# Kernel optimization log

Hardware: AMD Instinct MI355X
Metric: run time of the kernel (lower is better)

## Reference

```python
import jax, jax.numpy as jnp
import numpy as np

DIM = 1024
HEADS = 16
SCALE = DIM ** -0.5  # NOTE: original scales by full dim, not head dim


def setup_inputs() -> dict:
    key = jax.random.key(0)
    ks = jax.random.split(key, 6)
    B, S, D = 2, 2048, DIM
    x = jax.random.normal(ks[0], (B, S, D), dtype=jnp.float32)
    Wq = jax.random.normal(ks[1], (D, D), dtype=jnp.float32) * 0.02
    Wk = jax.random.normal(ks[2], (D, D), dtype=jnp.float32) * 0.02
    Wv = jax.random.normal(ks[3], (D, D), dtype=jnp.float32) * 0.02
    Wo = jax.random.normal(ks[4], (D, D), dtype=jnp.float32) * 0.02
    z = jnp.zeros((D,), dtype=jnp.float32)
    return {"x": x, "Wq": Wq, "bq": z, "Wk": Wk, "bk": z, "Wv": Wv, "bv": z, "Wo": Wo, "bo": z}


def reference(x, Wq, bq, Wk, bk, Wv, bv, Wo, bo):
    B, S, D = x.shape
    H = HEADS
    d = D // H
    # projections (Linear: x @ W + b)
    q = (x @ Wq + bq).reshape(B, S, H, d).transpose(0, 2, 1, 3)  # b h i d
    k = (x @ Wk + bk).reshape(B, S, H, d).transpose(0, 2, 1, 3)  # b h j d
    v = (x @ Wv + bv).reshape(B, S, H, d).transpose(0, 2, 1, 3)  # b h j d
    dots = jnp.einsum("bhid,bhjd->bhij", q, k) * SCALE
    # causal mask: strict upper triangle -> -inf
    mask = jnp.triu(jnp.ones((S, S), dtype=bool), k=1)
    dots = jnp.where(mask, -jnp.inf, dots)
    attn = jax.nn.softmax(dots, axis=-1)
    out = jnp.einsum("bhij,bhjd->bhid", attn, v)
    out = out.transpose(0, 2, 1, 3).reshape(B, S, D)  # b i (h d)
    return out @ Wo + bo
```

## Files before the change

### kernel.cpp

```cpp
#include <hip/hip_runtime.h>
#include <hip/hip_bf16.h>

typedef __bf16 bf16;
typedef __bf16 bf16x4 __attribute__((ext_vector_type(4)));
typedef __bf16 bf16x8 __attribute__((ext_vector_type(8)));
typedef float floatx4 __attribute__((ext_vector_type(4)));

#define MFMA_16x16x32(a, b, c) __builtin_amdgcn_mfma_f32_16x16x32_bf16((a), (b), (c), 0, 0, 0)
#define NEG_INF (-__builtin_inff())

#define CB 2
#define CS 2048
#define CD 1024
#define CH 16
#define CM (CB * CS)
#define QSC (0.03125f * 1.44269504088896340736f)

__device__ __forceinline__ void async16(const bf16* g, bf16* l) {
    __builtin_amdgcn_global_load_lds(
        (const __attribute__((address_space(1))) void*)g,
        (__attribute__((address_space(3))) void*)l, 16, 0, 0);
}

__global__ __launch_bounds__(256) void conv_x(const float* __restrict__ x,
                                              bf16* __restrict__ xb) {
    size_t i = ((size_t)blockIdx.x * 256 + threadIdx.x) * 8;
    float4 a = *(const float4*)(x + i);
    float4 b = *(const float4*)(x + i + 4);
    bf16x8 v;
    v[0] = (bf16)a.x; v[1] = (bf16)a.y; v[2] = (bf16)a.z; v[3] = (bf16)a.w;
    v[4] = (bf16)b.x; v[5] = (bf16)b.y; v[6] = (bf16)b.z; v[7] = (bf16)b.w;
    *(bf16x8*)(xb + i) = v;
}

__global__ __launch_bounds__(256) void conv_wt(
    const float* __restrict__ W0, const float* __restrict__ W1,
    const float* __restrict__ W2, const float* __restrict__ W3,
    bf16* __restrict__ Wt) {
    __shared__ bf16 Ws[64 * 68];
    const float* W = blockIdx.z == 0 ? W0 : blockIdx.z == 1 ? W1
                   : blockIdx.z == 2 ? W2 : W3;
    bf16* out = Wt + (size_t)blockIdx.z * CD * CD;
    const int t = threadIdx.x;
    const int n0 = blockIdx.x * 64, k0 = blockIdx.y * 64;
    const int rr = t >> 4, c4 = (t & 15) * 4;
#pragma unroll
    for (int i = 0; i < 4; i++) {
        int r = rr + i * 16;
        float4 f = *(const float4*)(W + (size_t)(k0 + r) * CD + n0 + c4);
        bf16x4 v;
        v[0] = (bf16)f.x; v[1] = (bf16)f.y; v[2] = (bf16)f.z; v[3] = (bf16)f.w;
        *(bf16x4*)&Ws[r * 68 + c4] = v;
    }
    __syncthreads();
#pragma unroll
    for (int i = 0; i < 4; i++) {
        int n = rr + i * 16;
        bf16x4 v;
#pragma unroll
        for (int j = 0; j < 4; j++) v[j] = Ws[(c4 + j) * 68 + n];
        *(bf16x4*)(out + (size_t)(n0 + n) * CD + k0 + c4) = v;
    }
}

__global__ __launch_bounds__(256) void gemm_qkv(
    const bf16* __restrict__ A, const bf16* __restrict__ Bt,
    const float* __restrict__ bq, const float* __restrict__ bk,
    const float* __restrict__ bv,
    bf16* __restrict__ Qb, bf16* __restrict__ Kb, bf16* __restrict__ Vb) {
    __shared__ bf16 As[128 * 32];
    __shared__ bf16 Bs[128 * 32];
    const int t = threadIdx.x, w = t >> 6, lane = t & 63;
    const int quad = lane >> 4, l15 = lane & 15;
    const int which = blockIdx.x >> 3;
    const int bn = (blockIdx.x & 7) * 128, bm = blockIdx.y * 128;
    const bf16* Bw = Bt + (size_t)which * CD * CD;

    const bf16* ag = A + (size_t)(bm + w * 16 + (lane >> 2)) * CD + (lane & 3) * 8;
    const bf16* bg = Bw + (size_t)(bn + w * 16 + (lane >> 2)) * CD + (lane & 3) * 8;
    const int lo = w * 16 * 32;

    const int wm = (w >> 1) * 64, wn = (w & 1) * 64;
    floatx4 acc[4][4] = {};

    for (int k0 = 0; k0 < CD; k0 += 32) {
        async16(ag + k0, &As[lo]);
        async16(ag + (size_t)64 * CD + k0, &As[lo + 64 * 32]);
        async16(bg + k0, &Bs[lo]);
        async16(bg + (size_t)64 * CD + k0, &Bs[lo + 64 * 32]);
        __syncthreads();
        bf16x8 af[4], bfr[4];
#pragma unroll
        for (int mt = 0; mt < 4; mt++)
            af[mt] = *(const bf16x8*)&As[(wm + mt * 16 + l15) * 32 + quad * 8];
#pragma unroll
        for (int nt = 0; nt < 4; nt++)
            bfr[nt] = *(const bf16x8*)&Bs[(wn + nt * 16 + l15) * 32 + quad * 8];
#pragma unroll
        for (int mt = 0; mt < 4; mt++)
#pragma unroll
            for (int nt = 0; nt < 4; nt++)
                acc[mt][nt] = MFMA_16x16x32(af[mt], bfr[nt], acc[mt][nt]);
        __syncthreads();
    }

    const float* bias = which == 0 ? bq : which == 1 ? bk : bv;
    bf16* out = which == 0 ? Qb : Kb;
#pragma unroll
    for (int mt = 0; mt < 4; mt++) {
#pragma unroll
        for (int nt = 0; nt < 4; nt++) {
            int token = bm + wm + mt * 16 + quad * 4;
            int col = bn + wn + nt * 16 + l15;
            int b = token >> 11, s = token & (CS - 1);
            int h = col >> 6, dd = col & 63;
            if (which == 2) {
                bf16x4 pv;
#pragma unroll
                for (int r = 0; r < 4; r++) pv[r] = (bf16)(acc[mt][nt][r] + bias[col]);
                *(bf16x4*)&Vb[(((size_t)(b * CH + h)) * 64 + dd) * CS + s] = pv;
            } else {
#pragma unroll
                for (int r = 0; r < 4; r++) {
                    float v = acc[mt][nt][r] + bias[col];
                    if (which == 0) v *= QSC;
                    out[(((size_t)(b * CH + h)) * CS + s + r) * 64 + dd] = (bf16)v;
                }
            }
        }
    }
}

__global__ __launch_bounds__(256) void gemm_o(
    const bf16* __restrict__ A, const bf16* __restrict__ Bt,
    const float* __restrict__ bias, float* __restrict__ out) {
    __shared__ bf16 As[64 * 32];
    __shared__ bf16 Bs[128 * 32];
    const int t = threadIdx.x, w = t >> 6, lane = t & 63;
    const int quad = lane >> 4, l15 = lane & 15;
    const int bn = blockIdx.x * 128, bm = blockIdx.y * 64;

    const bf16* ag = A + (size_t)(bm + w * 16 + (lane >> 2)) * CD + (lane & 3) * 8;
    const bf16* bg = Bt + (size_t)(bn + w * 16 + (lane >> 2)) * CD + (lane & 3) * 8;
    const int lo = w * 16 * 32;

    const int wm = (w >> 1) * 32, wn = (w & 1) * 64;
    floatx4 acc[2][4] = {};

    for (int k0 = 0; k0 < CD; k0 += 32) {
        async16(ag + k0, &As[lo]);
        async16(bg + k0, &Bs[lo]);
        async16(bg + (size_t)64 * CD + k0, &Bs[lo + 64 * 32]);
        __syncthreads();
        bf16x8 af[2], bfr[4];
#pragma unroll
        for (int mt = 0; mt < 2; mt++)
            af[mt] = *(const bf16x8*)&As[(wm + mt * 16 + l15) * 32 + quad * 8];
#pragma unroll
        for (int nt = 0; nt < 4; nt++)
            bfr[nt] = *(const bf16x8*)&Bs[(wn + nt * 16 + l15) * 32 + quad * 8];
#pragma unroll
        for (int mt = 0; mt < 2; mt++)
#pragma unroll
            for (int nt = 0; nt < 4; nt++)
                acc[mt][nt] = MFMA_16x16x32(af[mt], bfr[nt], acc[mt][nt]);
        __syncthreads();
    }

#pragma unroll
    for (int mt = 0; mt < 2; mt++)
#pragma unroll
        for (int nt = 0; nt < 4; nt++)
#pragma unroll
            for (int r = 0; r < 4; r++) {
                int row = bm + wm + mt * 16 + quad * 4 + r;
                int col = bn + wn + nt * 16 + l15;
                out[(size_t)row * CD + col] = acc[mt][nt][r] + bias[col];
            }
}

__global__ __launch_bounds__(256) void attn_kernel(
    const bf16* __restrict__ Q, const bf16* __restrict__ Kg,
    const bf16* __restrict__ Vg, bf16* __restrict__ Ob) {
    __shared__ bf16 Ks[64 * 72];
    __shared__ bf16 Vt[64 * 72];
    __shared__ bf16 Pt[4][32 * 72];

    const int t = threadIdx.x;
    const int w = t >> 6, lane = t & 63;
    const int quad = lane >> 4, l15 = lane & 15;

    const int half = blockIdx.x >> 8;
    const int slot = blockIdx.x & 255;
    const int bh   = slot & 31;
    const int qq   = slot >> 5;
    const int qb   = half ? qq : (15 - qq);
    const int q0   = qb * 128;
    const int wrow0 = q0 + w * 32;
    const int nT = 2 * qb + 2;

    const bf16* Qh = Q + (size_t)bh * CS * 64;
    const bf16* Kh = Kg + (size_t)bh * CS * 64;
    const bf16* Vh = Vg + (size_t)bh * 64 * CS;

    const int strow = t >> 2, soff = (t & 3) * 16;
    const bf16* ksrc = Kh + (size_t)strow * 64 + soff;
    const bf16* vsrc = Vh + (size_t)strow * CS + soff;

    bf16x8 kr0 = *(const bf16x8*)ksrc;
    bf16x8 kr1 = *(const bf16x8*)(ksrc + 8);
    bf16x8 vr0 = *(const bf16x8*)vsrc;
    bf16x8 vr1 = *(const bf16x8*)(vsrc + 8);

    bf16x8 qf[2][2];
#pragma unroll
    for (int g = 0; g < 2; g++) {
        const bf16* qsrc = Qh + (size_t)(wrow0 + g * 16 + l15) * 64 + quad * 8;
        qf[g][0] = *(const bf16x8*)qsrc;
        qf[g][1] = *(const bf16x8*)(qsrc + 32);
    }

    floatx4 o[4][2] = {};
    float m_r[2] = {NEG_INF, NEG_INF}, l_r[2] = {0.f, 0.f};

    bf16* pw = Pt[w];

    for (int kt = 0; kt < nT; kt++) {
        const int ks0 = kt * 64;
        __syncthreads();
        *(bf16x8*)&Ks[strow * 72 + soff]     = kr0;
        *(bf16x8*)&Ks[strow * 72 + soff + 8] = kr1;
        *(bf16x8*)&Vt[strow * 72 + soff]     = vr0;
        *(bf16x8*)&Vt[strow * 72 + soff + 8] = vr1;
        __syncthreads();
        {
            int nk = (kt + 1 < nT) ? kt + 1 : 0;
            const bf16* kn = ksrc + (size_t)nk * 64 * 64;
            const bf16* vn = vsrc + nk * 64;
            kr0 = *(const bf16x8*)kn;
            kr1 = *(const bf16x8*)(kn + 8);
            vr0 = *(const bf16x8*)vn;
            vr1 = *(const bf16x8*)(vn + 8);
        }
        if (ks0 > wrow0 + 31) continue;

        floatx4 sc[2][4] = {};
#pragma unroll
        for (int nt = 0; nt < 4; nt++) {
            bf16x8 af0 = *(const bf16x8*)&Ks[(nt * 16 + l15) * 72 + quad * 8];
            bf16x8 af1 = *(const bf16x8*)&Ks[(nt * 16 + l15) * 72 + 32 + quad * 8];
#pragma unroll
            for (int g = 0; g < 2; g++) {
                sc[g][nt] = MFMA_16x16x32(af0, qf[g][0], sc[g][nt]);
                sc[g][nt] = MFMA_16x16x32(af1, qf[g][1], sc[g][nt]);
            }
        }
        if (ks0 + 63 > wrow0) {
#pragma unroll
            for (int g = 0; g < 2; g++) {
                int qrow = wrow0 + g * 16 + l15;
#pragma unroll
                for (int nt = 0; nt < 4; nt++)
#pragma unroll
                    for (int r = 0; r < 4; r++)
                        if (ks0 + nt * 16 + quad * 4 + r > qrow)
                            sc[g][nt][r] = NEG_INF;
            }
        }
        float alpha_g[2];
#pragma unroll
        for (int g = 0; g < 2; g++) {
            float mx = NEG_INF;
#pragma unroll
            for (int nt = 0; nt < 4; nt++)
#pragma unroll
                for (int r = 0; r < 4; r++) mx = fmaxf(mx, sc[g][nt][r]);
            mx = fmaxf(mx, __shfl_xor(mx, 16));
            mx = fmaxf(mx, __shfl_xor(mx, 32));
            float mn = fmaxf(m_r[g], mx);
            alpha_g[g] = __builtin_amdgcn_exp2f(m_r[g] - mn);
            m_r[g] = mn;
            float sum = 0.f;
#pragma unroll
            for (int nt = 0; nt < 4; nt++)
#pragma unroll
                for (int r = 0; r < 4; r++) {
                    sc[g][nt][r] = __builtin_amdgcn_exp2f(sc[g][nt][r] - mn);
                    sum += sc[g][nt][r];
                }
            sum += __shfl_xor(sum, 16);
            sum += __shfl_xor(sum, 32);
            l_r[g] = l_r[g] * alpha_g[g] + sum;
        }
#pragma unroll
        for (int g = 0; g < 2; g++)
#pragma unroll
            for (int nt = 0; nt < 4; nt++) {
                bf16x4 pk;
#pragma unroll
                for (int r = 0; r < 4; r++) pk[r] = (bf16)sc[g][nt][r];
                *(bf16x4*)&pw[(g * 16 + l15) * 72 + nt * 16 + quad * 4] = pk;
            }
        bf16x8 bp[2][2];
#pragma unroll
        for (int g = 0; g < 2; g++) {
            bp[g][0] = *(const bf16x8*)&pw[(g * 16 + l15) * 72 + quad * 8];
            bp[g][1] = *(const bf16x8*)&pw[(g * 16 + l15) * 72 + 32 + quad * 8];
        }
#pragma unroll
        for (int dt = 0; dt < 4; dt++)
#pragma unroll
            for (int g = 0; g < 2; g++)
#pragma unroll
                for (int r = 0; r < 4; r++) o[dt][g][r] *= alpha_g[g];
#pragma unroll
        for (int dt = 0; dt < 4; dt++) {
            bf16x8 av0 = *(const bf16x8*)&Vt[(dt * 16 + l15) * 72 + quad * 8];
            bf16x8 av1 = *(const bf16x8*)&Vt[(dt * 16 + l15) * 72 + 32 + quad * 8];
#pragma unroll
            for (int g = 0; g < 2; g++) {
                o[dt][g] = MFMA_16x16x32(av0, bp[g][0], o[dt][g]);
                o[dt][g] = MFMA_16x16x32(av1, bp[g][1], o[dt][g]);
            }
        }
    }

    const int b = bh >> 4, h = bh & 15;
#pragma unroll
    for (int g = 0; g < 2; g++) {
        float rl = 1.f / l_r[g];
        int row = wrow0 + g * 16 + l15;
#pragma unroll
        for (int dt = 0; dt < 4; dt++) {
            bf16x4 ov;
#pragma unroll
            for (int r = 0; r < 4; r++) ov[r] = (bf16)(o[dt][g][r] * rl);
            *(bf16x4*)&Ob[((size_t)b * CS + row) * CD + h * 64 + dt * 16 + quad * 4] = ov;
        }
    }
}

extern "C" void kernel_launch(void* const* d_in, const int* in_sizes, int n_in,
                              void* d_out, int out_size, void* d_ws, size_t ws_size,
                              hipStream_t stream) {
    const float* x  = (const float*)d_in[0];
    const float* Wq = (const float*)d_in[1];
    const float* bq = (const float*)d_in[2];
    const float* Wk = (const float*)d_in[3];
    const float* bk = (const float*)d_in[4];
    const float* Wv = (const float*)d_in[5];
    const float* bv = (const float*)d_in[6];
    const float* Wo = (const float*)d_in[7];
    const float* bo = (const float*)d_in[8];
    float* out = (float*)d_out;

    bf16* xb = (bf16*)d_ws;
    bf16* Wt = xb + (size_t)CM * CD;
    bf16* Qb = Wt + (size_t)4 * CD * CD;
    bf16* Kb = Qb + (size_t)CB * CH * CS * 64;
    bf16* Vb = Kb + (size_t)CB * CH * CS * 64;
    bf16* Ob = Vb + (size_t)CB * CH * CS * 64;

    conv_x<<<(CM * CD) / (256 * 8), 256, 0, stream>>>(x, xb);
    conv_wt<<<dim3(CD / 64, CD / 64, 4), 256, 0, stream>>>(Wq, Wk, Wv, Wo, Wt);

    gemm_qkv<<<dim3(24, CM / 128), 256, 0, stream>>>(
        xb, Wt, bq, bk, bv, Qb, Kb, Vb);

    attn_kernel<<<512, 256, 0, stream>>>(Qb, Kb, Vb, Ob);

    gemm_o<<<dim3(8, CM / 64), 256, 0, stream>>>(
        Ob, Wt + (size_t)3 * CD * CD, bo, out);
}
```

Before: 194.4 us.

## Load attention K/V fragments directly into registers and vectorize GEMM epilogues

The attention kernel stops staging K and V tiles in shared memory with block-wide barriers. Each wave now loads its own MFMA fragments straight from global memory into registers, prefetching the next tile, and runs only up to its own causal limit. This removes the __syncthreads and lets waves proceed independently, at the cost of more redundant global/L2 traffic because every wave reloads the same K/V. The QKV and output GEMMs swap the MFMA operand order so the epilogue can write contiguous 4-element vectors with float4 bias loads, and the attention kernel gets a launch_bounds occupancy hint of 2.

```diff
diff --git a/kernel.cpp b/kernel.cpp
--- a/kernel.cpp
+++ b/kernel.cpp
@@ -75,6 +75,7 @@
     const int which = blockIdx.x >> 3;
     const int bn = (blockIdx.x & 7) * 128, bm = blockIdx.y * 128;
     const bf16* Bw = Bt + (size_t)which * CD * CD;
+    const bool vpath = (which == 2);
 
     const bf16* ag = A + (size_t)(bm + w * 16 + (lane >> 2)) * CD + (lane & 3) * 8;
     const bf16* bg = Bw + (size_t)(bn + w * 16 + (lane >> 2)) * CD + (lane & 3) * 8;
@@ -96,38 +97,57 @@
 #pragma unroll
         for (int nt = 0; nt < 4; nt++)
             bfr[nt] = *(const bf16x8*)&Bs[(wn + nt * 16 + l15) * 32 + quad * 8];
+        if (vpath) {
+#pragma unroll
+            for (int mt = 0; mt < 4; mt++)
+#pragma unroll
+                for (int nt = 0; nt < 4; nt++)
+                    acc[mt][nt] = MFMA_16x16x32(af[mt], bfr[nt], acc[mt][nt]);
+        } else {
+#pragma unroll
+            for (int mt = 0; mt < 4; mt++)
+#pragma unroll
+                for (int nt = 0; nt < 4; nt++)
+                    acc[mt][nt] = MFMA_16x16x32(bfr[nt], af[mt], acc[mt][nt]);
+        }
+        __syncthreads();
+    }
+
+    if (vpath) {
 #pragma unroll
         for (int mt = 0; mt < 4; mt++)
 #pragma unroll
-            for (int nt = 0; nt < 4; nt++)
-                acc[mt][nt] = MFMA_16x16x32(af[mt], bfr[nt], acc[mt][nt]);
-        __syncthreads();
-    }
-
-    const float* bias = which == 0 ? bq : which == 1 ? bk : bv;
-    bf16* out = which == 0 ? Qb : Kb;
-#pragma unroll
-    for (int mt = 0; mt < 4; mt++) {
-#pragma unroll
-        for (int nt = 0; nt < 4; nt++) {
-            int token = bm + wm + mt * 16 + quad * 4;
-            int col = bn + wn + nt * 16 + l15;
-            int b = token >> 11, s = token & (CS - 1);
-            int h = col >> 6, dd = col & 63;
-            if (which == 2) {
+            for (int nt = 0; nt < 4; nt++) {
+                int token = bm + wm + mt * 16 + quad * 4;
+                int col = bn + wn + nt * 16 + l15;
+                int b = token >> 11, s = token & (CS - 1);
+                int h = col >> 6, dd = col & 63;
                 bf16x4 pv;
 #pragma unroll
-                for (int r = 0; r < 4; r++) pv[r] = (bf16)(acc[mt][nt][r] + bias[col]);
+                for (int r = 0; r < 4; r++) pv[r] = (bf16)(acc[mt][nt][r] + bv[col]);
                 *(bf16x4*)&Vb[(((size_t)(b * CH + h)) * 64 + dd) * CS + s] = pv;
-            } else {
+            }
+    } else {
+        const float* bias = which == 0 ? bq : bk;
+        bf16* out = which == 0 ? Qb : Kb;
+#pragma unroll
+        for (int mt = 0; mt < 4; mt++)
+#pragma unroll
+            for (int nt = 0; nt < 4; nt++) {
+                int token = bm + wm + mt * 16 + l15;
+                int f = bn + wn + nt * 16 + quad * 4;
+                int b = token >> 11, s = token & (CS - 1);
+                int h = f >> 6, dd = f & 63;
+                float4 bb = *(const float4*)(bias + f);
+                bf16x4 pv;
 #pragma unroll
                 for (int r = 0; r < 4; r++) {
-                    float v = acc[mt][nt][r] + bias[col];
+                    float v = acc[mt][nt][r] + ((const float*)&bb)[r];
                     if (which == 0) v *= QSC;
-                    out[(((size_t)(b * CH + h)) * CS + s + r) * 64 + dd] = (bf16)v;
+                    pv[r] = (bf16)v;
                 }
-            }
-        }
+                *(bf16x4*)&out[(((size_t)(b * CH + h)) * CS + s) * 64 + dd] = pv;
+            }
     }
 }
 
@@ -163,27 +183,29 @@
         for (int mt = 0; mt < 2; mt++)
 #pragma unroll
             for (int nt = 0; nt < 4; nt++)
-                acc[mt][nt] = MFMA_16x16x32(af[mt], bfr[nt], acc[mt][nt]);
+                acc[mt][nt] = MFMA_16x16x32(bfr[nt], af[mt], acc[mt][nt]);
         __syncthreads();
     }
 
 #pragma unroll
     for (int mt = 0; mt < 2; mt++)
 #pragma unroll
-        for (int nt = 0; nt < 4; nt++)
-#pragma unroll
-            for (int r = 0; r < 4; r++) {
-                int row = bm + wm + mt * 16 + quad * 4 + r;
-                int col = bn + wn + nt * 16 + l15;
-                out[(size_t)row * CD + col] = acc[mt][nt][r] + bias[col];
-            }
-}
-
-__global__ __launch_bounds__(256) void attn_kernel(
+        for (int nt = 0; nt < 4; nt++) {
+            int token = bm + wm + mt * 16 + l15;
+            int f = bn + wn + nt * 16 + quad * 4;
+            float4 bb = *(const float4*)(bias + f);
+            float4 ov;
+            ov.x = acc[mt][nt][0] + bb.x;
+            ov.y = acc[mt][nt][1] + bb.y;
+            ov.z = acc[mt][nt][2] + bb.z;
+            ov.w = acc[mt][nt][3] + bb.w;
+            *(float4*)&out[(size_t)token * CD + f] = ov;
+        }
+}
+
+__global__ __launch_bounds__(256, 2) void attn_kernel(
     const bf16* __restrict__ Q, const bf16* __restrict__ Kg,
     const bf16* __restrict__ Vg, bf16* __restrict__ Ob) {
-    __shared__ bf16 Ks[64 * 72];
-    __shared__ bf16 Vt[64 * 72];
     __shared__ bf16 Pt[4][32 * 72];
 
     const int t = threadIdx.x;
@@ -197,20 +219,11 @@
     const int qb   = half ? qq : (15 - qq);
     const int q0   = qb * 128;
     const int wrow0 = q0 + w * 32;
-    const int nT = 2 * qb + 2;
+    const int ktmax = (wrow0 + 31) >> 6;
 
     const bf16* Qh = Q + (size_t)bh * CS * 64;
     const bf16* Kh = Kg + (size_t)bh * CS * 64;
     const bf16* Vh = Vg + (size_t)bh * 64 * CS;
-
-    const int strow = t >> 2, soff = (t & 3) * 16;
-    const bf16* ksrc = Kh + (size_t)strow * 64 + soff;
-    const bf16* vsrc = Vh + (size_t)strow * CS + soff;
-
-    bf16x8 kr0 = *(const bf16x8*)ksrc;
-    bf16x8 kr1 = *(const bf16x8*)(ksrc + 8);
-    bf16x8 vr0 = *(const bf16x8*)vsrc;
-    bf16x8 vr1 = *(const bf16x8*)(vsrc + 8);
 
     bf16x8 qf[2][2];
 #pragma unroll
@@ -220,42 +233,44 @@
         qf[g][1] = *(const bf16x8*)(qsrc + 32);
     }
 
+    const bf16* kfb = Kh + (size_t)l15 * 64 + quad * 8;
+    const bf16* vfb = Vh + (size_t)l15 * CS + quad * 8;
+
+    bf16x8 ka[4][2], va[4][2];
+#pragma unroll
+    for (int nt = 0; nt < 4; nt++) {
+        ka[nt][0] = *(const bf16x8*)(kfb + nt * 1024);
+        ka[nt][1] = *(const bf16x8*)(kfb + nt * 1024 + 32);
+    }
+#pragma unroll
+    for (int dt = 0; dt < 4; dt++) {
+        va[dt][0] = *(const bf16x8*)(vfb + (size_t)dt * 16 * CS);
+        va[dt][1] = *(const bf16x8*)(vfb + (size_t)dt * 16 * CS + 32);
+    }
+
     floatx4 o[4][2] = {};
     float m_r[2] = {NEG_INF, NEG_INF}, l_r[2] = {0.f, 0.f};
-
     bf16* pw = Pt[w];
 
-    for (int kt = 0; kt < nT; kt++) {
+    for (int kt = 0; kt <= ktmax; kt++) {
         const int ks0 = kt * 64;
-        __syncthreads();
-        *(bf16x8*)&Ks[strow * 72 + soff]     = kr0;
-        *(bf16x8*)&Ks[strow * 72 + soff + 8] = kr1;
-        *(bf16x8*)&Vt[strow * 72 + soff]     = vr0;
-        *(bf16x8*)&Vt[strow * 72 + soff + 8] = vr1;
-        __syncthreads();
-        {
-            int nk = (kt + 1 < nT) ? kt + 1 : 0;
-            const bf16* kn = ksrc + (size_t)nk * 64 * 64;
-            const bf16* vn = vsrc + nk * 64;
-            kr0 = *(const bf16x8*)kn;
-            kr1 = *(const bf16x8*)(kn + 8);
-            vr0 = *(const bf16x8*)vn;
-            vr1 = *(const bf16x8*)(vn + 8);
-        }
-        if (ks0 > wrow0 + 31) continue;
-
         floatx4 sc[2][4] = {};
 #pragma unroll
-        for (int nt = 0; nt < 4; nt++) {
-            bf16x8 af0 = *(const bf16x8*)&Ks[(nt * 16 + l15) * 72 + quad * 8];
-            bf16x8 af1 = *(const bf16x8*)&Ks[(nt * 16 + l15) * 72 + 32 + quad * 8];
+        for (int nt = 0; nt < 4; nt++)
 #pragma unroll
             for (int g = 0; g < 2; g++) {
-                sc[g][nt] = MFMA_16x16x32(af0, qf[g][0], sc[g][nt]);
-                sc[g][nt] = MFMA_16x16x32(af1, qf[g][1], sc[g][nt]);
-            }
-        }
-        if (ks0 + 63 > wrow0) {
+                sc[g][nt] = MFMA_16x16x32(ka[nt][0], qf[g][0], sc[g][nt]);
+                sc[g][nt] = MFMA_16x16x32(ka[nt][1], qf[g][1], sc[g][nt]);
+            }
+        if (kt < ktmax) {
+            const bf16* kn = kfb + (size_t)(ks0 + 64) * 64;
+#pragma unroll
+            for (int nt = 0; nt < 4; nt++) {
+                ka[nt][0] = *(const bf16x8*)(kn + nt * 1024);
+                ka[nt][1] = *(const bf16x8*)(kn + nt * 1024 + 32);
+            }
+        }
+        if (kt == ktmax) {
 #pragma unroll
             for (int g = 0; g < 2; g++) {
                 int qrow = wrow0 + g * 16 + l15;
@@ -314,13 +329,18 @@
 #pragma unroll
                 for (int r = 0; r < 4; r++) o[dt][g][r] *= alpha_g[g];
 #pragma unroll
-        for (int dt = 0; dt < 4; dt++) {
-            bf16x8 av0 = *(const bf16x8*)&Vt[(dt * 16 + l15) * 72 + quad * 8];
-            bf16x8 av1 = *(const bf16x8*)&Vt[(dt * 16 + l15) * 72 + 32 + quad * 8];
+        for (int dt = 0; dt < 4; dt++)
 #pragma unroll
             for (int g = 0; g < 2; g++) {
-                o[dt][g] = MFMA_16x16x32(av0, bp[g][0], o[dt][g]);
-                o[dt][g] = MFMA_16x16x32(av1, bp[g][1], o[dt][g]);
+                o[dt][g] = MFMA_16x16x32(va[dt][0], bp[g][0], o[dt][g]);
+                o[dt][g] = MFMA_16x16x32(va[dt][1], bp[g][1], o[dt][g]);
+            }
+        if (kt < ktmax) {
+            const bf16* vn = vfb + ks0 + 64;
+#pragma unroll
+            for (int dt = 0; dt < 4; dt++) {
+                va[dt][0] = *(const bf16x8*)(vn + (size_t)dt * 16 * CS);
+                va[dt][1] = *(const bf16x8*)(vn + (size_t)dt * 16 * CS + 32);
             }
         }
     }
```

Result: slower. 241.4 us (+24.2%).
